# Kernel optimization log

Hardware: AMD Instinct MI355X
Metric: run time of the kernel (lower is better)

Reference implementation:

```python
import jax, jax.numpy as jnp
import numpy as np

C, N, E = 256, 256, 2048          # subgraphs, nodes/subgraph, edges/subgraph
F_IN, NHID, DDI = 128, 128, 256
K1, K2, K3 = 128, 64, 32          # top-k sizes for pooling_ratio=0.5
P, B = 16, 16                     # DAG hierarchy: P parents x B leaf children
GN = C + P + 1                    # global DAG nodes (leaves + parents + root)
GE = 8192                         # global pos/neg edge count


def setup_inputs():
    key = jax.random.key(0)
    ks = jax.random.split(key, 16)
    inp = {
        "x": jax.random.normal(ks[0], (C, N, F_IN), jnp.float32),
        "edge_index": jax.random.randint(ks[1], (C, 2, E), 0, N),
        "edge_weight": jax.random.uniform(ks[2], (C, E), dtype=jnp.float32),
        "global_edge_index": jax.random.randint(ks[3], (2, GE), 0, GN),
        "neg_edge_index": jax.random.randint(ks[4], (2, GE), 0, GN),
    }
    names = [("W1", F_IN, NHID), ("Wp1", NHID, 1), ("W2", NHID, NHID),
             ("Wp2", NHID, 1), ("W3", NHID, NHID), ("Wp3", NHID, 1),
             ("Wg", 6 * NHID, DDI), ("Wl1", DDI, DDI), ("Wl2", DDI, DDI)]
    for i, (nm, fi, fo) in enumerate(names):
        inp[nm] = jax.random.normal(ks[5 + i], (fi, fo), jnp.float32) / np.sqrt(fi)
        inp["b" + nm[1:]] = jnp.zeros((fo,), jnp.float32)
    return inp


def gcn(x, ei, ew, W, b):
    """PyG GCNConv with self-loops: D^-1/2 (A+I) D^-1/2 X W + b."""
    n = x.shape[0]
    h = x @ W
    row, col = ei[0], ei[1]
    deg = 1.0 + jax.ops.segment_sum(ew, col, num_segments=n)
    dis = jax.lax.rsqrt(deg)
    norm = dis[row] * ew * dis[col]                       # [E]
    agg = jax.ops.segment_sum(norm[:, None] * h[row], col, num_segments=n)
    return agg + h / deg[:, None] + b


def sag_pool(x, ei, ew, Ws, bs, k):
    """SAGPooling: GCN score, per-graph top-k, gate by tanh(score), edge filter."""
    n = x.shape[0]
    score = gcn(x, ei, ew, Ws, bs)[:, 0]
    vals, perm = jax.lax.top_k(score, k)
    x_new = x[perm] * jnp.tanh(vals)[:, None]
    newid = jnp.full((n,), -1, jnp.int32).at[perm].set(jnp.arange(k, dtype=jnp.int32))
    r, c = newid[ei[0]], newid[ei[1]]
    keep = (r >= 0) & (c >= 0)
    ei_new = jnp.where(keep, jnp.stack([r, c]), 0)        # dropped edges -> node 0
    ew_new = jnp.where(keep, ew, 0.0)                     # with zero weight
    return x_new, ei_new, ew_new


def _subgraph(x, ei, ew, W1, b1, Wp1, bp1, W2, b2, Wp2, bp2, W3, b3, Wp3, bp3):
    x = jax.nn.relu(gcn(x, ei, ew, W1, b1))
    x, ei, ew = sag_pool(x, ei, ew, Wp1, bp1, K1)
    x1 = jnp.concatenate([x.max(0), x.mean(0)])           # gmp||gap, batch all-zero
    x = jax.nn.relu(gcn(x, ei, ew, W2, b2))
    x, ei, ew = sag_pool(x, ei, ew, Wp2, bp2, K2)
    x2 = jnp.concatenate([x.max(0), x.mean(0)])
    x = jax.nn.relu(gcn(x, ei, ew, W3, b3))
    x, ei, ew = sag_pool(x, ei, ew, Wp3, bp3, K3)
    x3 = jnp.concatenate([x.max(0), x.mean(0)])
    return jnp.concatenate([x1, x2, x3])                  # [6*NHID]


def reference(x, edge_index, edge_weight, global_edge_index, neg_edge_index,
              W1, b1, Wp1, bp1, W2, b2, Wp2, bp2, W3, b3, Wp3, bp3,
              Wg, bg, Wl1, bl1, Wl2, bl2):
    # per-class subgraph pipeline, vmapped over the C subgraphs
    leaf = jax.vmap(_subgraph, in_axes=(0, 0, 0) + (None,) * 12)(
        x, edge_index, edge_weight,
        W1, b1, Wp1, bp1, W2, b2, Wp2, bp2, W3, b3, Wp3, bp3)   # [C, 6*NHID]
    # Get_Fs: mean-aggregate children features up the DAG (fixed 2-level + root)
    parent = leaf.reshape(P, B, -1).mean(axis=1)                # [P, 6*NHID]
    root = parent.mean(axis=0, keepdims=True)                   # [1, 6*NHID]
    gfeat = jnp.concatenate([leaf, parent, root], axis=0)       # [GN, 6*NHID]
    # global GCN (unit edge weights)
    gx = jax.nn.relu(gcn(gfeat, global_edge_index,
                         jnp.ones((GE,), gfeat.dtype), Wg, bg)) # [GN, DDI]
    class_embedding = gx[:C]
    # feature_split + lin1/lin2 + dot-product scores
    pos_s = gx[global_edge_index[0]] @ Wl1 + bl1
    pos_t = gx[global_edge_index[1]] @ Wl2 + bl2
    neg_s = gx[neg_edge_index[0]] @ Wl1 + bl1
    neg_t = gx[neg_edge_index[1]] @ Wl2 + bl2
    pos = jnp.sum(pos_s * pos_t, axis=1)
    neg = jnp.sum(neg_s * neg_t, axis=1)
    # BCEWithLogits: targets 1 for pos, 0 for neg
    loss = jnp.mean(jax.nn.softplus(-pos)) + jnp.mean(jax.nn.softplus(neg))
    return class_embedding, loss
```

## Files before the change

kernel.cpp:

```cpp
#include <hip/hip_runtime.h>
#include <math.h>

#define NT 1024
#define EDGES 2048
#define SENT 0xFFFF

struct SmemA {
  float xbuf[256 * 128];
  unsigned short rc[EDGES];
  float ewl[EDGES];
  unsigned short csr_row[EDGES];
  float csr_coef[EDGES];
  float degs[256];
  float diss[256];
  int   csr_off[257];
  int   csr_cnt[256];
  float hsv[256];
  float scorev[256];
  float vals[128];
  short perm[128];
  signed char newid[256];
};

__device__ __forceinline__ float4* xvec(float* xb, int row, int c4) {
  return reinterpret_cast<float4*>(xb + (row << 7) + ((c4 ^ (row & 7)) << 2));
}
__device__ __forceinline__ int xidx(int row, int col) {
  return (row << 7) + ((((col >> 2) ^ (row & 7)) << 2) | (col & 3));
}

template<int NN, int K, bool FIRST, bool REMAP>
__device__ __forceinline__ void run_stage(
    SmemA& sm,
    const float* __restrict__ xg,
    const int* __restrict__ eic,
    const float* __restrict__ ewc,
    const float* __restrict__ W,
    const float* __restrict__ b,
    const float* __restrict__ Wp,
    const float* __restrict__ bp,
    float& lmax, float& lmean)
{
  constexpr int NPT  = NN / 64;
  constexpr int Q    = NN / 64;
  constexpr int SEG  = NT / NN;
  constexpr int LEN  = NN / SEG;
  constexpr int LOG  = (NN == 256) ? 8 : (NN == 128 ? 7 : 6);
  const int tid  = threadIdx.x;
  const int lane = tid & 63;
  const int fbase = __builtin_amdgcn_readfirstlane((tid >> 6) << 3);
  const int c4b   = fbase >> 2;

  if (FIRST) {
    if (tid < NN) { sm.degs[tid] = 1.0f; sm.csr_cnt[tid] = 0; }
    __syncthreads();
    const float4* xg4 = reinterpret_cast<const float4*>(xg);
    for (int i = tid; i < 256 * 32; i += NT) {
      const float4 v = xg4[i];
      *xvec(sm.xbuf, i >> 5, i & 31) = v;
    }
    for (int e = tid; e < EDGES; e += NT) {
      const int row = eic[e], col = eic[EDGES + e];
      const float w = ewc[e];
      sm.rc[e]  = (unsigned short)((row << 8) | col);
      sm.ewl[e] = w;
      atomicAdd(&sm.degs[col], w);
      atomicAdd(&sm.csr_cnt[col], 1);
    }
    __syncthreads();
  }

  if (tid < NN) sm.diss[tid] = rsqrtf(sm.degs[tid]);
  if (tid < 64) {
    int c[Q], pre[Q];
    int tot = 0;
#pragma unroll
    for (int i = 0; i < Q; i++) { c[i] = sm.csr_cnt[tid * Q + i]; pre[i] = tot; tot += c[i]; }
    int inc = tot;
#pragma unroll
    for (int d = 1; d < 64; d <<= 1) {
      const int o = __shfl_up(inc, d, 64);
      if (tid >= d) inc += o;
    }
    const int base = inc - tot;
    if (tid == 0) sm.csr_off[0] = 0;
#pragma unroll
    for (int i = 0; i < Q; i++) {
      sm.csr_off[tid * Q + i + 1] = base + pre[i] + c[i];
      sm.csr_cnt[tid * Q + i] = 0;
    }
  }
  __syncthreads();

  if (tid < NN) { sm.hsv[tid] = 0.0f; sm.scorev[tid] = 0.0f; }
  for (int e = tid; e < EDGES; e += NT) {
    const unsigned short r = sm.rc[e];
    if (FIRST || r != SENT) {
      const int row = r >> 8, col = r & 255;
      const int p = atomicAdd(&sm.csr_cnt[col], 1);
      const int s = sm.csr_off[col] + p;
      sm.csr_row[s]  = (unsigned short)row;
      sm.csr_coef[s] = sm.diss[row] * sm.ewl[e];
    }
  }
  __syncthreads();

  float acc[NPT][8];
#pragma unroll
  for (int i = 0; i < NPT; i++)
#pragma unroll
    for (int j = 0; j < 8; j++) acc[i][j] = 0.0f;

#pragma unroll 4
  for (int k4 = 0; k4 < 32; k4++) {
    float4 xv[NPT];
#pragma unroll
    for (int i = 0; i < NPT; i++) xv[i] = *xvec(sm.xbuf, lane + (i << 6), k4);
#pragma unroll
    for (int kk = 0; kk < 4; kk++) {
      const float* wr = W + (((k4 << 2) + kk) << 7) + fbase;
      const float4 wa = *reinterpret_cast<const float4*>(wr);
      const float4 wb = *reinterpret_cast<const float4*>(wr + 4);
      const float wv[8] = {wa.x, wa.y, wa.z, wa.w, wb.x, wb.y, wb.z, wb.w};
#pragma unroll
      for (int i = 0; i < NPT; i++) {
        const float xs = (kk == 0) ? xv[i].x : (kk == 1) ? xv[i].y : (kk == 2) ? xv[i].z : xv[i].w;
#pragma unroll
        for (int j = 0; j < 8; j++) acc[i][j] = fmaf(xs, wv[j], acc[i][j]);
      }
    }
  }
  __syncthreads();

#pragma unroll
  for (int i = 0; i < NPT; i++) {
    const int v = lane + (i << 6);
    *xvec(sm.xbuf, v, c4b)     = make_float4(acc[i][0], acc[i][1], acc[i][2], acc[i][3]);
    *xvec(sm.xbuf, v, c4b + 1) = make_float4(acc[i][4], acc[i][5], acc[i][6], acc[i][7]);
  }
  __syncthreads();

  {
    const float4 ba = *reinterpret_cast<const float4*>(b + fbase);
    const float4 bb = *reinterpret_cast<const float4*>(b + fbase + 4);
    const float bv[8] = {ba.x, ba.y, ba.z, ba.w, bb.x, bb.y, bb.z, bb.w};
    const float4 wa = *reinterpret_cast<const float4*>(Wp + fbase);
    const float4 wb = *reinterpret_cast<const float4*>(Wp + fbase + 4);
    const float wv[8] = {wa.x, wa.y, wa.z, wa.w, wb.x, wb.y, wb.z, wb.w};
#pragma unroll
    for (int i = 0; i < NPT; i++) {
      const int v = lane + (i << 6);
      const int beg = sm.csr_off[v], end = sm.csr_off[v + 1];
      float ag[8] = {0.f, 0.f, 0.f, 0.f, 0.f, 0.f, 0.f, 0.f};
      float4 plo = make_float4(0.f, 0.f, 0.f, 0.f), phi = plo;
      float cf_nxt = 0.0f;
      if (beg < end) {
        const int r0 = sm.csr_row[beg];
        cf_nxt = sm.csr_coef[beg];
        plo = *xvec(sm.xbuf, r0, c4b);
        phi = *xvec(sm.xbuf, r0, c4b + 1);
      }
      for (int s = beg; s < end; ++s) {
        const float4 lo = plo, hi = phi;
        const float cf = cf_nxt;
        if (s + 1 < end) {
          const int rn = sm.csr_row[s + 1];
          cf_nxt = sm.csr_coef[s + 1];
          plo = *xvec(sm.xbuf, rn, c4b);
          phi = *xvec(sm.xbuf, rn, c4b + 1);
        }
        ag[0] = fmaf(cf, lo.x, ag[0]); ag[1] = fmaf(cf, lo.y, ag[1]);
        ag[2] = fmaf(cf, lo.z, ag[2]); ag[3] = fmaf(cf, lo.w, ag[3]);
        ag[4] = fmaf(cf, hi.x, ag[4]); ag[5] = fmaf(cf, hi.y, ag[5]);
        ag[6] = fmaf(cf, hi.z, ag[6]); ag[7] = fmaf(cf, hi.w, ag[7]);
      }
      const float dv = sm.diss[v];
      const float invd = 1.0f / sm.degs[v];
      float part = 0.0f;
#pragma unroll
      for (int j = 0; j < 8; j++) {
        acc[i][j] = fmaxf(fmaf(ag[j], dv, fmaf(acc[i][j], invd, bv[j])), 0.0f);
        part = fmaf(acc[i][j], wv[j], part);
      }
      atomicAdd(&sm.hsv[v], part);
    }
  }
  __syncthreads();

#pragma unroll
  for (int i = 0; i < NPT; i++) {
    const int v = lane + (i << 6);
    *xvec(sm.xbuf, v, c4b)     = make_float4(acc[i][0], acc[i][1], acc[i][2], acc[i][3]);
    *xvec(sm.xbuf, v, c4b + 1) = make_float4(acc[i][4], acc[i][5], acc[i][6], acc[i][7]);
  }
  for (int e = tid; e < EDGES; e += NT) {
    const unsigned short r = sm.rc[e];
    if (FIRST || r != SENT) {
      const int row = r >> 8, col = r & 255;
      atomicAdd(&sm.scorev[col], sm.diss[row] * sm.ewl[e] * sm.hsv[row]);
    }
  }
  __syncthreads();
  if (tid < NN) {
    sm.scorev[tid] = sm.scorev[tid] * sm.diss[tid] + sm.hsv[tid] / sm.degs[tid] + bp[0];
    sm.csr_cnt[tid] = 0;
  }
  __syncthreads();

  {
    const int node = tid & (NN - 1);
    const int seg  = tid >> LOG;
    const float sv = sm.scorev[node];
    int part = 0;
    const int u0 = seg * LEN;
#pragma unroll 4
    for (int u = u0; u < u0 + LEN; u++) {
      const float su = sm.scorev[u];
      part += (su > sv) || (su == sv && u < node);
    }
    if (part) atomicAdd(&sm.csr_cnt[node], part);
  }
  __syncthreads();
  if (tid < NN) {
    const int rank = sm.csr_cnt[tid];
    if (rank < K) { sm.perm[rank] = (short)tid; sm.vals[rank] = sm.scorev[tid]; sm.newid[tid] = (signed char)rank; }
    else sm.newid[tid] = -1;
    if (tid < K) { sm.degs[tid] = 1.0f; sm.csr_cnt[tid] = 0; }
  }
  __syncthreads();

  {
    constexpr int TPR = NT / K;
    constexpr int C4  = 32 / TPR;
    const int drow = tid / TPR;
    const int cc   = (tid % TPR) * C4;
    const int src  = sm.perm[drow];
    const float g  = tanhf(sm.vals[drow]);
    float4 tmp[C4];
#pragma unroll
    for (int j = 0; j < C4; j++) tmp[j] = *xvec(sm.xbuf, src, cc + j);
    __syncthreads();
#pragma unroll
    for (int j = 0; j < C4; j++) {
      tmp[j].x *= g; tmp[j].y *= g; tmp[j].z *= g; tmp[j].w *= g;
      *xvec(sm.xbuf, drow, cc + j) = tmp[j];
    }
  }
  __syncthreads();

  if (tid < 128) {
    float mx = -INFINITY, sv = 0.0f;
    for (int i = 0; i < K; i++) {
      const float v = sm.xbuf[xidx(i, tid)];
      mx = fmaxf(mx, v); sv += v;
    }
    lmax = mx;
    lmean = sv * (1.0f / K);
  }
  if (REMAP) {
    for (int e = tid; e < EDGES; e += NT) {
      const unsigned short r = sm.rc[e];
      if (FIRST || r != SENT) {
        const int r2 = sm.newid[r >> 8];
        const int c2 = sm.newid[r & 255];
        if (r2 < 0 || c2 < 0) sm.rc[e] = SENT;
        else {
          sm.rc[e] = (unsigned short)((r2 << 8) | c2);
          atomicAdd(&sm.degs[c2], sm.ewl[e]);
          atomicAdd(&sm.csr_cnt[c2], 1);
        }
      }
    }
  }
  __syncthreads();
}

__global__ __launch_bounds__(NT)
void stageA_kernel(const float* __restrict__ x0,
                   const int* __restrict__ ei, const float* __restrict__ ew,
                   const float* __restrict__ W1, const float* __restrict__ b1,
                   const float* __restrict__ Wp1, const float* __restrict__ bp1,
                   const float* __restrict__ W2, const float* __restrict__ b2,
                   const float* __restrict__ Wp2, const float* __restrict__ bp2,
                   const float* __restrict__ W3, const float* __restrict__ b3,
                   const float* __restrict__ Wp3, const float* __restrict__ bp3,
                   const float* __restrict__ Wg, float* __restrict__ hG)
{
  __shared__ SmemA sm;
  const int c = blockIdx.x;
  const int tid = threadIdx.x;
  if (c == 0 && tid < 256) hG[(size_t)272 * 256 + tid] = 0.0f;
  const int* eic = ei + (size_t)c * 2 * EDGES;
  const float* ewc = ew + (size_t)c * EDGES;
  const float* xgc = x0 + (size_t)c * 256 * 128;
  float l0 = 0.f, l1 = 0.f, l2 = 0.f, l3 = 0.f, l4 = 0.f, l5 = 0.f;
  run_stage<256, 128, true,  true >(sm, xgc, eic, ewc, W1, b1, Wp1, bp1, l0, l1);
  run_stage<128,  64, false, true >(sm, nullptr, nullptr, nullptr, W2, b2, Wp2, bp2, l2, l3);
  run_stage< 64,  32, false, false>(sm, nullptr, nullptr, nullptr, W3, b3, Wp3, bp3, l4, l5);

  float* leafbuf = sm.csr_coef;
  float* hGacc   = sm.degs;
  if (tid < 256) {
    if (tid < 128) {
      leafbuf[tid]       = l0; leafbuf[128 + tid] = l1;
      leafbuf[256 + tid] = l2; leafbuf[384 + tid] = l3;
      leafbuf[512 + tid] = l4; leafbuf[640 + tid] = l5;
    }
    hGacc[tid] = 0.0f;
  }
  __syncthreads();
  {
    const int f = tid & 255, q = tid >> 8;
    const float* wgq = Wg + (size_t)(q * 192) * 256 + f;
    const float* lb  = leafbuf + q * 192;
    float p0 = 0.f, p1 = 0.f, p2 = 0.f, p3 = 0.f;
    for (int i = 0; i < 192; i += 4) {
      p0 = fmaf(lb[i],     wgq[(size_t)i * 256],       p0);
      p1 = fmaf(lb[i + 1], wgq[(size_t)(i + 1) * 256], p1);
      p2 = fmaf(lb[i + 2], wgq[(size_t)(i + 2) * 256], p2);
      p3 = fmaf(lb[i + 3], wgq[(size_t)(i + 3) * 256], p3);
    }
    atomicAdd(&hGacc[f], (p0 + p1) + (p2 + p3));
  }
  __syncthreads();
  if (tid < 256) hG[(size_t)c * 256 + tid] = hGacc[tid];
}

__global__ __launch_bounds__(NT)
void prep_k(float* __restrict__ hG, const int* __restrict__ gei,
            float* __restrict__ degG, int* __restrict__ goff,
            int* __restrict__ gcsr_row, float* __restrict__ gcsr_coef,
            float* __restrict__ lacc, int* __restrict__ lctr) {
  const int tid = threadIdx.x;
  if (blockIdx.x == 16) {
    __shared__ int cnt[320];
    __shared__ int off[321];
    __shared__ int fc[288];
    for (int i = tid; i < 320; i += NT) cnt[i] = 0;
    if (tid < 288) fc[tid] = 0;
    __syncthreads();
    for (int e = tid; e < 8192; e += NT) atomicAdd(&cnt[gei[8192 + e]], 1);
    __syncthreads();
    if (tid < 64) {
      int cc[5], pre[5];
      int tot = 0;
#pragma unroll
      for (int i = 0; i < 5; i++) { cc[i] = cnt[tid * 5 + i]; pre[i] = tot; tot += cc[i]; }
      int inc = tot;
#pragma unroll
      for (int d = 1; d < 64; d <<= 1) {
        const int o = __shfl_up(inc, d, 64);
        if (tid >= d) inc += o;
      }
      const int base = inc - tot;
      if (tid == 0) off[0] = 0;
#pragma unroll
      for (int i = 0; i < 5; i++) off[tid * 5 + i + 1] = base + pre[i] + cc[i];
    }
    if (tid < 273) degG[tid] = 1.0f + (float)cnt[tid];
    __syncthreads();
    for (int e = tid; e < 8192; e += NT) {
      const int col = gei[8192 + e], row = gei[e];
      const int p = atomicAdd(&fc[col], 1);
      const int s = off[col] + p;
      gcsr_row[s]  = row;
      gcsr_coef[s] = rsqrtf(1.0f + (float)cnt[row]);
    }
    if (tid < 274) goff[tid] = off[tid];
    if (tid == 0) { *lacc = 0.0f; *lctr = 0; }
    return;
  }
  __shared__ float pr[1024];
  const int p = blockIdx.x;
  const int f = tid & 255, q = tid >> 8;
  float s = 0.f;
  for (int b2 = q; b2 < 16; b2 += 4) s += hG[(size_t)(p * 16 + b2) * 256 + f];
  pr[tid] = s;
  __syncthreads();
  if (tid < 256) {
    const float sv = (pr[tid] + pr[256 + tid] + pr[512 + tid] + pr[768 + tid]) * (1.0f / 16.0f);
    hG[(size_t)(256 + p) * 256 + tid] = sv;
    atomicAdd(&hG[(size_t)272 * 256 + tid], sv * (1.0f / 16.0f));
  }
}

__global__ __launch_bounds__(NT)
void gaggemb_k(const float* __restrict__ hG, const float* __restrict__ degG,
               const int* __restrict__ goff, const int* __restrict__ gcsr_row,
               const float* __restrict__ gcsr_coef, const float* __restrict__ bg,
               const float* __restrict__ Wl1, const float* __restrict__ bl1,
               const float* __restrict__ Wl2, const float* __restrict__ bl2,
               float* __restrict__ out_ce, float* __restrict__ A,
               float* __restrict__ B) {
  __shared__ float pacc[1024];
  __shared__ float pacc2[1024];
  __shared__ float gxr[256];
  const int v = blockIdx.x, tid = threadIdx.x;
  const int f = tid & 255, q = tid >> 8;
  {
    const int beg = goff[v], end = goff[v + 1];
    float s = 0.f;
    for (int i = beg + q; i < end; i += 4)
      s = fmaf(gcsr_coef[i], hG[(size_t)gcsr_row[i] * 256 + f], s);
    pacc[tid] = s;
  }
  __syncthreads();
  if (tid < 256) {
    const float dg = degG[v];
    float val = (pacc[tid] + pacc[256 + tid] + pacc[512 + tid] + pacc[768 + tid]) * rsqrtf(dg)
              + hG[(size_t)v * 256 + tid] / dg + bg[tid];
    val = fmaxf(val, 0.0f);
    gxr[tid] = val;
    if (v < 256) out_ce[(size_t)v * 256 + tid] = val;
  }
  __syncthreads();
  {
    const int k0 = q << 6;
    float a = 0.f, b2 = 0.f;
    for (int k = k0; k < k0 + 64; k++) {
      const float g = gxr[k];
      a  = fmaf(g, Wl1[(size_t)k * 256 + f], a);
      b2 = fmaf(g, Wl2[(size_t)k * 256 + f], b2);
    }
    pacc[tid] = a; pacc2[tid] = b2;
  }
  __syncthreads();
  if (tid < 256) {
    A[(size_t)v * 256 + tid] = pacc[tid] + pacc[256 + tid] + pacc[512 + tid] + pacc[768 + tid] + bl1[tid];
    B[(size_t)v * 256 + tid] = pacc2[tid] + pacc2[256 + tid] + pacc2[512 + tid] + pacc2[768 + tid] + bl2[tid];
  }
}

__global__ __launch_bounds__(256)
void loss_k(const float* __restrict__ A, const float* __restrict__ B,
            const int* __restrict__ gei, const int* __restrict__ nei,
            float* __restrict__ acc, int* __restrict__ lctr,
            float* __restrict__ out) {
  const int gw = (blockIdx.x * blockDim.x + threadIdx.x) >> 6;
  const int lane = threadIdx.x & 63;
  float lsum = 0.0f;
  for (int idx = gw; idx < 16384; idx += 512) {
    const bool ispos = idx < 8192;
    const int e = ispos ? idx : idx - 8192;
    const int* ia = ispos ? gei : nei;
    const int s = ia[e], t = ia[8192 + e];
    float p = 0.0f;
#pragma unroll
    for (int j = 0; j < 4; j++)
      p += A[(size_t)s * 256 + lane + 64 * j] * B[(size_t)t * 256 + lane + 64 * j];
#pragma unroll
    for (int off = 32; off; off >>= 1) p += __shfl_xor(p, off, 64);
    const float z = ispos ? -p : p;
    lsum += fmaxf(z, 0.0f) + log1pf(expf(-fabsf(z)));
  }
  if (lane == 0) atomicAdd(acc, lsum);
  __syncthreads();
  if (threadIdx.x == 0) {
    __threadfence();
    const int old = atomicAdd(lctr, 1);
    if (old == (int)gridDim.x - 1) {
      const float tot = atomicAdd(acc, 0.0f);
      out[65536] = tot * (1.0f / 8192.0f);
    }
  }
}

extern "C" void kernel_launch(void* const* d_in, const int* in_sizes, int n_in,
                              void* d_out, int out_size, void* d_ws, size_t ws_size,
                              hipStream_t stream) {
  const float* x   = (const float*)d_in[0];
  const int*   ei  = (const int*)d_in[1];
  const float* ew  = (const float*)d_in[2];
  const int*   gei = (const int*)d_in[3];
  const int*   nei = (const int*)d_in[4];
  const float* W1  = (const float*)d_in[5];
  const float* b1  = (const float*)d_in[6];
  const float* Wp1 = (const float*)d_in[7];
  const float* bp1 = (const float*)d_in[8];
  const float* W2  = (const float*)d_in[9];
  const float* b2  = (const float*)d_in[10];
  const float* Wp2 = (const float*)d_in[11];
  const float* bp2 = (const float*)d_in[12];
  const float* W3  = (const float*)d_in[13];
  const float* b3  = (const float*)d_in[14];
  const float* Wp3 = (const float*)d_in[15];
  const float* bp3 = (const float*)d_in[16];
  const float* Wg  = (const float*)d_in[17];
  const float* bg  = (const float*)d_in[18];
  const float* Wl1 = (const float*)d_in[19];
  const float* bl1 = (const float*)d_in[20];
  const float* Wl2 = (const float*)d_in[21];
  const float* bl2 = (const float*)d_in[22];

  float* ws       = (float*)d_ws;
  float* hG       = ws;
  float* degG     = hG + 273 * 256;
  float* Aemb     = degG + 288;
  float* Bemb     = Aemb + 273 * 256;
  float* lacc     = Bemb + 273 * 256;
  int*   lctr     = (int*)(lacc + 1);
  int*   goff     = lctr + 1;
  int*   gcsr_row = goff + 288;
  float* gcsr_coef= (float*)(gcsr_row + 8192);
  float* out      = (float*)d_out;

  stageA_kernel<<<256, NT, 0, stream>>>(x, ei, ew, W1, b1, Wp1, bp1,
                                        W2, b2, Wp2, bp2, W3, b3, Wp3, bp3,
                                        Wg, hG);
  prep_k<<<17, NT, 0, stream>>>(hG, gei, degG, goff, gcsr_row, gcsr_coef,
                                lacc, lctr);
  gaggemb_k<<<273, NT, 0, stream>>>(hG, degG, goff, gcsr_row, gcsr_coef, bg,
                                    Wl1, bl1, Wl2, bl2, out, Aemb, Bemb);
  loss_k<<<128, 256, 0, stream>>>(Aemb, Bemb, gei, nei, lacc, lctr, out);
}
```

Baseline: 187.2 us.

## Widen per-thread feature tile to 16 and move global CSR build into stage A

Each wave now owns 16 output features instead of 8, and the 16 waves split into two row groups, so each thread reads each activation from LDS once for twice as many FMAs. This raises register use and idles half the lanes when a stage has 64 nodes. The global-graph CSR construction moves out of prep_k into an extra block of stageA_kernel, so it runs alongside the subgraph work and no longer delays the parent/root aggregation kernel.

```diff
diff --git a/kernel.cpp b/kernel.cpp
--- a/kernel.cpp
+++ b/kernel.cpp
@@ -41,15 +41,20 @@
     const float* __restrict__ bp,
     float& lmax, float& lmean)
 {
-  constexpr int NPT  = NN / 64;
   constexpr int Q    = NN / 64;
   constexpr int SEG  = NT / NN;
   constexpr int LEN  = NN / SEG;
   constexpr int LOG  = (NN == 256) ? 8 : (NN == 128 ? 7 : 6);
+  constexpr int NPT  = (NN == 256) ? 2 : 1;
   const int tid  = threadIdx.x;
   const int lane = tid & 63;
-  const int fbase = __builtin_amdgcn_readfirstlane((tid >> 6) << 3);
+  const int wid  = tid >> 6;
+  const int fbase = __builtin_amdgcn_readfirstlane((wid & 7) << 4);
   const int c4b   = fbase >> 2;
+  const int rg    = wid >> 3;
+  const int rbase = rg * (NN / 2);
+  const bool act  = (NN > 64) || (lane < 32);
+  const int lrow  = (NN == 64) ? (lane & 31) : lane;
 
   if (FIRST) {
     if (tid < NN) { sm.degs[tid] = 1.0f; sm.csr_cnt[tid] = 0; }
@@ -105,93 +110,116 @@
   }
   __syncthreads();
 
-  float acc[NPT][8];
+  float acc[NPT][16];
 #pragma unroll
   for (int i = 0; i < NPT; i++)
 #pragma unroll
-    for (int j = 0; j < 8; j++) acc[i][j] = 0.0f;
-
-#pragma unroll 4
+    for (int j = 0; j < 16; j++) acc[i][j] = 0.0f;
+
+#pragma unroll 2
   for (int k4 = 0; k4 < 32; k4++) {
     float4 xv[NPT];
 #pragma unroll
-    for (int i = 0; i < NPT; i++) xv[i] = *xvec(sm.xbuf, lane + (i << 6), k4);
+    for (int i = 0; i < NPT; i++) xv[i] = *xvec(sm.xbuf, rbase + lrow + (i << 6), k4);
 #pragma unroll
     for (int kk = 0; kk < 4; kk++) {
       const float* wr = W + (((k4 << 2) + kk) << 7) + fbase;
       const float4 wa = *reinterpret_cast<const float4*>(wr);
       const float4 wb = *reinterpret_cast<const float4*>(wr + 4);
-      const float wv[8] = {wa.x, wa.y, wa.z, wa.w, wb.x, wb.y, wb.z, wb.w};
+      const float4 wc = *reinterpret_cast<const float4*>(wr + 8);
+      const float4 wd = *reinterpret_cast<const float4*>(wr + 12);
+      const float wv[16] = {wa.x, wa.y, wa.z, wa.w, wb.x, wb.y, wb.z, wb.w,
+                            wc.x, wc.y, wc.z, wc.w, wd.x, wd.y, wd.z, wd.w};
 #pragma unroll
       for (int i = 0; i < NPT; i++) {
         const float xs = (kk == 0) ? xv[i].x : (kk == 1) ? xv[i].y : (kk == 2) ? xv[i].z : xv[i].w;
 #pragma unroll
-        for (int j = 0; j < 8; j++) acc[i][j] = fmaf(xs, wv[j], acc[i][j]);
+        for (int j = 0; j < 16; j++) acc[i][j] = fmaf(xs, wv[j], acc[i][j]);
       }
     }
   }
   __syncthreads();
 
-#pragma unroll
-  for (int i = 0; i < NPT; i++) {
-    const int v = lane + (i << 6);
-    *xvec(sm.xbuf, v, c4b)     = make_float4(acc[i][0], acc[i][1], acc[i][2], acc[i][3]);
-    *xvec(sm.xbuf, v, c4b + 1) = make_float4(acc[i][4], acc[i][5], acc[i][6], acc[i][7]);
+  if (act) {
+#pragma unroll
+    for (int i = 0; i < NPT; i++) {
+      const int v = rbase + lrow + (i << 6);
+      *xvec(sm.xbuf, v, c4b)     = make_float4(acc[i][0],  acc[i][1],  acc[i][2],  acc[i][3]);
+      *xvec(sm.xbuf, v, c4b + 1) = make_float4(acc[i][4],  acc[i][5],  acc[i][6],  acc[i][7]);
+      *xvec(sm.xbuf, v, c4b + 2) = make_float4(acc[i][8],  acc[i][9],  acc[i][10], acc[i][11]);
+      *xvec(sm.xbuf, v, c4b + 3) = make_float4(acc[i][12], acc[i][13], acc[i][14], acc[i][15]);
+    }
   }
   __syncthreads();
 
   {
     const float4 ba = *reinterpret_cast<const float4*>(b + fbase);
     const float4 bb = *reinterpret_cast<const float4*>(b + fbase + 4);
-    const float bv[8] = {ba.x, ba.y, ba.z, ba.w, bb.x, bb.y, bb.z, bb.w};
+    const float4 bc = *reinterpret_cast<const float4*>(b + fbase + 8);
+    const float4 bd = *reinterpret_cast<const float4*>(b + fbase + 12);
+    const float bv[16] = {ba.x, ba.y, ba.z, ba.w, bb.x, bb.y, bb.z, bb.w,
+                          bc.x, bc.y, bc.z, bc.w, bd.x, bd.y, bd.z, bd.w};
     const float4 wa = *reinterpret_cast<const float4*>(Wp + fbase);
     const float4 wb = *reinterpret_cast<const float4*>(Wp + fbase + 4);
-    const float wv[8] = {wa.x, wa.y, wa.z, wa.w, wb.x, wb.y, wb.z, wb.w};
+    const float4 wc = *reinterpret_cast<const float4*>(Wp + fbase + 8);
+    const float4 wd = *reinterpret_cast<const float4*>(Wp + fbase + 12);
+    const float wv[16] = {wa.x, wa.y, wa.z, wa.w, wb.x, wb.y, wb.z, wb.w,
+                          wc.x, wc.y, wc.z, wc.w, wd.x, wd.y, wd.z, wd.w};
 #pragma unroll
     for (int i = 0; i < NPT; i++) {
-      const int v = lane + (i << 6);
+      const int v = rbase + lrow + (i << 6);
       const int beg = sm.csr_off[v], end = sm.csr_off[v + 1];
-      float ag[8] = {0.f, 0.f, 0.f, 0.f, 0.f, 0.f, 0.f, 0.f};
-      float4 plo = make_float4(0.f, 0.f, 0.f, 0.f), phi = plo;
+      float ag[16];
+#pragma unroll
+      for (int j = 0; j < 16; j++) ag[j] = 0.0f;
+      float4 p0 = make_float4(0.f,0.f,0.f,0.f), p1 = p0, p2 = p0, p3 = p0;
       float cf_nxt = 0.0f;
       if (beg < end) {
         const int r0 = sm.csr_row[beg];
         cf_nxt = sm.csr_coef[beg];
-        plo = *xvec(sm.xbuf, r0, c4b);
-        phi = *xvec(sm.xbuf, r0, c4b + 1);
+        p0 = *xvec(sm.xbuf, r0, c4b);     p1 = *xvec(sm.xbuf, r0, c4b + 1);
+        p2 = *xvec(sm.xbuf, r0, c4b + 2); p3 = *xvec(sm.xbuf, r0, c4b + 3);
       }
       for (int s = beg; s < end; ++s) {
-        const float4 lo = plo, hi = phi;
+        const float4 q0 = p0, q1 = p1, q2 = p2, q3 = p3;
         const float cf = cf_nxt;
         if (s + 1 < end) {
           const int rn = sm.csr_row[s + 1];
           cf_nxt = sm.csr_coef[s + 1];
-          plo = *xvec(sm.xbuf, rn, c4b);
-          phi = *xvec(sm.xbuf, rn, c4b + 1);
+          p0 = *xvec(sm.xbuf, rn, c4b);     p1 = *xvec(sm.xbuf, rn, c4b + 1);
+          p2 = *xvec(sm.xbuf, rn, c4b + 2); p3 = *xvec(sm.xbuf, rn, c4b + 3);
         }
-        ag[0] = fmaf(cf, lo.x, ag[0]); ag[1] = fmaf(cf, lo.y, ag[1]);
-        ag[2] = fmaf(cf, lo.z, ag[2]); ag[3] = fmaf(cf, lo.w, ag[3]);
-        ag[4] = fmaf(cf, hi.x, ag[4]); ag[5] = fmaf(cf, hi.y, ag[5]);
-        ag[6] = fmaf(cf, hi.z, ag[6]); ag[7] = fmaf(cf, hi.w, ag[7]);
+        ag[0]  = fmaf(cf, q0.x, ag[0]);  ag[1]  = fmaf(cf, q0.y, ag[1]);
+        ag[2]  = fmaf(cf, q0.z, ag[2]);  ag[3]  = fmaf(cf, q0.w, ag[3]);
+        ag[4]  = fmaf(cf, q1.x, ag[4]);  ag[5]  = fmaf(cf, q1.y, ag[5]);
+        ag[6]  = fmaf(cf, q1.z, ag[6]);  ag[7]  = fmaf(cf, q1.w, ag[7]);
+        ag[8]  = fmaf(cf, q2.x, ag[8]);  ag[9]  = fmaf(cf, q2.y, ag[9]);
+        ag[10] = fmaf(cf, q2.z, ag[10]); ag[11] = fmaf(cf, q2.w, ag[11]);
+        ag[12] = fmaf(cf, q3.x, ag[12]); ag[13] = fmaf(cf, q3.y, ag[13]);
+        ag[14] = fmaf(cf, q3.z, ag[14]); ag[15] = fmaf(cf, q3.w, ag[15]);
       }
       const float dv = sm.diss[v];
       const float invd = 1.0f / sm.degs[v];
       float part = 0.0f;
 #pragma unroll
-      for (int j = 0; j < 8; j++) {
+      for (int j = 0; j < 16; j++) {
         acc[i][j] = fmaxf(fmaf(ag[j], dv, fmaf(acc[i][j], invd, bv[j])), 0.0f);
         part = fmaf(acc[i][j], wv[j], part);
       }
-      atomicAdd(&sm.hsv[v], part);
-    }
-  }
-  __syncthreads();
-
-#pragma unroll
-  for (int i = 0; i < NPT; i++) {
-    const int v = lane + (i << 6);
-    *xvec(sm.xbuf, v, c4b)     = make_float4(acc[i][0], acc[i][1], acc[i][2], acc[i][3]);
-    *xvec(sm.xbuf, v, c4b + 1) = make_float4(acc[i][4], acc[i][5], acc[i][6], acc[i][7]);
+      if (act) atomicAdd(&sm.hsv[v], part);
+    }
+  }
+  __syncthreads();
+
+  if (act) {
+#pragma unroll
+    for (int i = 0; i < NPT; i++) {
+      const int v = rbase + lrow + (i << 6);
+      *xvec(sm.xbuf, v, c4b)     = make_float4(acc[i][0],  acc[i][1],  acc[i][2],  acc[i][3]);
+      *xvec(sm.xbuf, v, c4b + 1) = make_float4(acc[i][4],  acc[i][5],  acc[i][6],  acc[i][7]);
+      *xvec(sm.xbuf, v, c4b + 2) = make_float4(acc[i][8],  acc[i][9],  acc[i][10], acc[i][11]);
+      *xvec(sm.xbuf, v, c4b + 3) = make_float4(acc[i][12], acc[i][13], acc[i][14], acc[i][15]);
+    }
   }
   for (int e = tid; e < EDGES; e += NT) {
     const unsigned short r = sm.rc[e];
@@ -278,17 +306,61 @@
 __global__ __launch_bounds__(NT)
 void stageA_kernel(const float* __restrict__ x0,
                    const int* __restrict__ ei, const float* __restrict__ ew,
+                   const int* __restrict__ gei,
                    const float* __restrict__ W1, const float* __restrict__ b1,
                    const float* __restrict__ Wp1, const float* __restrict__ bp1,
                    const float* __restrict__ W2, const float* __restrict__ b2,
                    const float* __restrict__ Wp2, const float* __restrict__ bp2,
                    const float* __restrict__ W3, const float* __restrict__ b3,
                    const float* __restrict__ Wp3, const float* __restrict__ bp3,
-                   const float* __restrict__ Wg, float* __restrict__ hG)
+                   const float* __restrict__ Wg, float* __restrict__ hG,
+                   float* __restrict__ degG, int* __restrict__ goff,
+                   int* __restrict__ gcsr_row, float* __restrict__ gcsr_coef,
+                   float* __restrict__ lacc, int* __restrict__ lctr)
 {
   __shared__ SmemA sm;
   const int c = blockIdx.x;
   const int tid = threadIdx.x;
+
+  if (c == 256) {
+    int* cnt = (int*)sm.xbuf;
+    int* off = cnt + 320;
+    int* fc  = off + 321;
+    for (int i = tid; i < 320; i += NT) cnt[i] = 0;
+    if (tid < 288) fc[tid] = 0;
+    __syncthreads();
+    for (int e = tid; e < 8192; e += NT) atomicAdd(&cnt[gei[8192 + e]], 1);
+    __syncthreads();
+    if (tid < 64) {
+      int cc[5], pre[5];
+      int tot = 0;
+#pragma unroll
+      for (int i = 0; i < 5; i++) { cc[i] = cnt[tid * 5 + i]; pre[i] = tot; tot += cc[i]; }
+      int inc = tot;
+#pragma unroll
+      for (int d = 1; d < 64; d <<= 1) {
+        const int o = __shfl_up(inc, d, 64);
+        if (tid >= d) inc += o;
+      }
+      const int base = inc - tot;
+      if (tid == 0) off[0] = 0;
+#pragma unroll
+      for (int i = 0; i < 5; i++) off[tid * 5 + i + 1] = base + pre[i] + cc[i];
+    }
+    if (tid < 273) degG[tid] = 1.0f + (float)cnt[tid];
+    __syncthreads();
+    for (int e = tid; e < 8192; e += NT) {
+      const int col = gei[8192 + e], row = gei[e];
+      const int p = atomicAdd(&fc[col], 1);
+      const int s = off[col] + p;
+      gcsr_row[s]  = row;
+      gcsr_coef[s] = rsqrtf(1.0f + (float)cnt[row]);
+    }
+    if (tid < 274) goff[tid] = off[tid];
+    if (tid == 0) { *lacc = 0.0f; *lctr = 0; }
+    return;
+  }
+
   if (c == 0 && tid < 256) hG[(size_t)272 * 256 + tid] = 0.0f;
   const int* eic = ei + (size_t)c * 2 * EDGES;
   const float* ewc = ew + (size_t)c * EDGES;
@@ -327,50 +399,9 @@
 }
 
 __global__ __launch_bounds__(NT)
-void prep_k(float* __restrict__ hG, const int* __restrict__ gei,
-            float* __restrict__ degG, int* __restrict__ goff,
-            int* __restrict__ gcsr_row, float* __restrict__ gcsr_coef,
-            float* __restrict__ lacc, int* __restrict__ lctr) {
+void prep_k(float* __restrict__ hG) {
+  __shared__ float pr[1024];
   const int tid = threadIdx.x;
-  if (blockIdx.x == 16) {
-    __shared__ int cnt[320];
-    __shared__ int off[321];
-    __shared__ int fc[288];
-    for (int i = tid; i < 320; i += NT) cnt[i] = 0;
-    if (tid < 288) fc[tid] = 0;
-    __syncthreads();
-    for (int e = tid; e < 8192; e += NT) atomicAdd(&cnt[gei[8192 + e]], 1);
-    __syncthreads();
-    if (tid < 64) {
-      int cc[5], pre[5];
-      int tot = 0;
-#pragma unroll
-      for (int i = 0; i < 5; i++) { cc[i] = cnt[tid * 5 + i]; pre[i] = tot; tot += cc[i]; }
-      int inc = tot;
-#pragma unroll
-      for (int d = 1; d < 64; d <<= 1) {
-        const int o = __shfl_up(inc, d, 64);
-        if (tid >= d) inc += o;
-      }
-      const int base = inc - tot;
-      if (tid == 0) off[0] = 0;
-#pragma unroll
-      for (int i = 0; i < 5; i++) off[tid * 5 + i + 1] = base + pre[i] + cc[i];
-    }
-    if (tid < 273) degG[tid] = 1.0f + (float)cnt[tid];
-    __syncthreads();
-    for (int e = tid; e < 8192; e += NT) {
-      const int col = gei[8192 + e], row = gei[e];
-      const int p = atomicAdd(&fc[col], 1);
-      const int s = off[col] + p;
-      gcsr_row[s]  = row;
-      gcsr_coef[s] = rsqrtf(1.0f + (float)cnt[row]);
-    }
-    if (tid < 274) goff[tid] = off[tid];
-    if (tid == 0) { *lacc = 0.0f; *lctr = 0; }
-    return;
-  }
-  __shared__ float pr[1024];
   const int p = blockIdx.x;
   const int f = tid & 255, q = tid >> 8;
   float s = 0.f;
@@ -504,11 +535,11 @@
   float* gcsr_coef= (float*)(gcsr_row + 8192);
   float* out      = (float*)d_out;
 
-  stageA_kernel<<<256, NT, 0, stream>>>(x, ei, ew, W1, b1, Wp1, bp1,
+  stageA_kernel<<<257, NT, 0, stream>>>(x, ei, ew, gei, W1, b1, Wp1, bp1,
                                         W2, b2, Wp2, bp2, W3, b3, Wp3, bp3,
-                                        Wg, hG);
-  prep_k<<<17, NT, 0, stream>>>(hG, gei, degG, goff, gcsr_row, gcsr_coef,
-                                lacc, lctr);
+                                        Wg, hG, degG, goff, gcsr_row, gcsr_coef,
+                                        lacc, lctr);
+  prep_k<<<16, NT, 0, stream>>>(hG);
   gaggemb_k<<<273, NT, 0, stream>>>(hG, degG, goff, gcsr_row, gcsr_coef, bg,
                                     Wl1, bl1, Wl2, bl2, out, Aemb, Bemb);
   loss_k<<<128, 256, 0, stream>>>(Aemb, Bemb, gei, nei, lacc, lctr, out);
```

After: 180.8 us (median of 2 runs). -3.4%, faster.
